# Kernel optimization log

Measured on AMD Instinct MI355X. Metric: run time of the kernel, lower is better.

The kernel has to match this reference:

```python
import jax, jax.numpy as jnp
import numpy as np

D_MODEL, N_HEADS, D_FF = 768, 12, 3072
D_HEAD = D_MODEL // N_HEADS
EPS = 1e-5


def layer_norm(x, g, b):
    mu = jnp.mean(x, axis=-1, keepdims=True)
    var = jnp.mean(jnp.square(x - mu), axis=-1, keepdims=True)
    return (x - mu) * jax.lax.rsqrt(var + EPS) * g + b


def setup_inputs() -> dict:
    key = jax.random.key(0)
    ks = jax.random.split(key, 8)
    B, T = 4, 2048
    s_in = 1.0 / np.sqrt(D_MODEL)
    s_ff = 1.0 / np.sqrt(D_FF)
    return {
        "x": jax.random.normal(ks[0], (B, T, D_MODEL), dtype=jnp.float32),
        "ln1_g": jnp.ones((D_MODEL,), jnp.float32),
        "ln1_b": jnp.zeros((D_MODEL,), jnp.float32),
        "qkv_w": jax.random.normal(ks[1], (D_MODEL, 3 * D_MODEL), jnp.float32) * s_in,
        "qkv_b": jnp.zeros((3 * D_MODEL,), jnp.float32),
        "attn_out_w": jax.random.normal(ks[2], (D_MODEL, D_MODEL), jnp.float32) * s_in,
        "attn_out_b": jnp.zeros((D_MODEL,), jnp.float32),
        "ln2_g": jnp.ones((D_MODEL,), jnp.float32),
        "ln2_b": jnp.zeros((D_MODEL,), jnp.float32),
        "ff1_w": jax.random.normal(ks[3], (D_MODEL, D_FF), jnp.float32) * s_in,
        "ff1_b": jnp.zeros((D_FF,), jnp.float32),
        "ff2_w": jax.random.normal(ks[4], (D_FF, D_MODEL), jnp.float32) * s_ff,
        "ff2_b": jnp.zeros((D_MODEL,), jnp.float32),
    }


def reference(x, ln1_g, ln1_b, qkv_w, qkv_b, attn_out_w, attn_out_b,
              ln2_g, ln2_b, ff1_w, ff1_b, ff2_w, ff2_b):
    B, T, D = x.shape
    h = layer_norm(x, ln1_g, ln1_b)
    qkv = h @ qkv_w + qkv_b                       # [B,T,3D]
    q, k, v = jnp.split(qkv, 3, axis=-1)
    def heads(t):  # [B,T,D] -> [B,H,T,dh]
        return t.reshape(B, T, N_HEADS, D_HEAD).transpose(0, 2, 1, 3)
    q, k, v = heads(q), heads(k), heads(v)
    scores = jnp.einsum('bhqd,bhkd->bhqk', q, k) / np.sqrt(D_HEAD)
    attn = jnp.einsum('bhqk,bhkd->bhqd', jax.nn.softmax(scores, axis=-1), v)
    attn = attn.transpose(0, 2, 1, 3).reshape(B, T, D)
    x = x + attn @ attn_out_w + attn_out_b
    h = layer_norm(x, ln2_g, ln2_b)
    ff = jax.nn.gelu(h @ ff1_w + ff1_b, approximate=True) @ ff2_w + ff2_b
    return x + ff
```

## Files before the change

### kernel.cpp

```cpp
#include <hip/hip_runtime.h>
#include <stdint.h>

typedef unsigned short ushort_t;
typedef unsigned int uint_t;

typedef __bf16 bf16x8 __attribute__((ext_vector_type(8)));
typedef float f32x4 __attribute__((ext_vector_type(4)));

#define DM 768
#define DFF 3072
#define NH 12
#define DH 64
#define TLEN 2048
#define BATCH 4
#define NROWS (BATCH * TLEN)
#define QKVW (3 * DM)
#define STG ((size_t)NROWS * DM)

#if __has_builtin(__builtin_amdgcn_exp2f)
#define EXP2(x) __builtin_amdgcn_exp2f(x)
#else
extern "C" __device__ float __ocml_native_exp2_f32(float);
#define EXP2(x) __ocml_native_exp2_f32(x)
#endif

__device__ __forceinline__ float b2f(ushort_t u) {
  union { uint_t i; float f; } c; c.i = ((uint_t)u) << 16; return c.f;
}
__device__ __forceinline__ ushort_t f2b(float f) {
  union { float f; uint_t i; } c; c.f = f;
  uint_t i = c.i;
  return (ushort_t)((i + 0x7fffu + ((i >> 16) & 1u)) >> 16);
}

__device__ __forceinline__ void gl_lds16(const ushort_t* g, ushort_t* l) {
  __builtin_amdgcn_global_load_lds(
      (const __attribute__((address_space(1))) uint_t*)g,
      (__attribute__((address_space(3))) uint_t*)l, 16, 0, 0);
}

__device__ __forceinline__ float gelu_f(float x) {
  float x2 = x * x;
  float c2n = -x * __builtin_fmaf(0.10294323f, x2, 2.3022082f);
  float t = EXP2(c2n);
  return x * __builtin_amdgcn_rcpf(1.0f + t);
}

__global__ __launch_bounds__(256) void detect_dtype(const ushort_t* __restrict__ x,
                                                    int* __restrict__ flag) {
  __shared__ int cnt[256];
  int c = 0;
  for (int i = threadIdx.x; i < 65536; i += 256)
    c += ((x[i] & 0x7F80u) == 0x7F80u) ? 1 : 0;
  cnt[threadIdx.x] = c;
  __syncthreads();
  for (int s = 128; s >= 1; s >>= 1) {
    if (threadIdx.x < s) cnt[threadIdx.x] += cnt[threadIdx.x + s];
    __syncthreads();
  }
  if (threadIdx.x == 0) flag[0] = (cnt[0] > 0) ? 1 : 0;
}

__global__ __launch_bounds__(256) void cvt_smalls(
    const void* s0, const void* s1, const void* s2, const void* s3,
    const void* s4, const void* s5, const void* s6, const void* s7,
    ushort_t* __restrict__ dst, const int* __restrict__ flag) {
  int f = flag[0];
  int i = blockIdx.x * 256 + threadIdx.x;
  if (i >= 9984) return;
  const void* src; int off;
  if (i < 768)       { src = s0; off = i; }
  else if (i < 1536) { src = s1; off = i - 768; }
  else if (i < 3840) { src = s2; off = i - 1536; }
  else if (i < 4608) { src = s3; off = i - 3840; }
  else if (i < 5376) { src = s4; off = i - 4608; }
  else if (i < 6144) { src = s5; off = i - 5376; }
  else if (i < 9216) { src = s6; off = i - 6144; }
  else               { src = s7; off = i - 9216; }
  dst[i] = f ? f2b(((const float*)src)[off]) : ((const ushort_t*)src)[off];
}

__global__ __launch_bounds__(256) void transpose_adapt(
    const void* __restrict__ inbase, long long inOff, ushort_t* __restrict__ out,
    int R, int C, int ldIn, const int* __restrict__ flag) {
  __shared__ alignas(16) ushort_t tile[32][33];
  int f = flag[0];
  const float* in32 = (const float*)inbase + inOff;
  const ushort_t* in16 = (const ushort_t*)inbase + inOff;
  int tc = blockIdx.x * 32, tr = blockIdx.y * 32;
  int lx = threadIdx.x & 31, ly = threadIdx.x >> 5;
#pragma unroll
  for (int i = 0; i < 32; i += 8) {
    size_t idx = (size_t)(tr + ly + i) * ldIn + tc + lx;
    tile[ly + i][lx] = f ? f2b(in32[idx]) : in16[idx];
  }
  __syncthreads();
#pragma unroll
  for (int i = 0; i < 32; i += 8)
    out[(size_t)(tc + ly + i) * R + tr + lx] = tile[lx][ly + i];
}

template <bool RAW>
__global__ __launch_bounds__(256) void ln_kernel(
    const void* __restrict__ xr, const ushort_t* __restrict__ g,
    const ushort_t* __restrict__ b, ushort_t* __restrict__ out,
    const int* __restrict__ flag) {
  int row = blockIdx.x * 4 + (threadIdx.x >> 6);
  int lane = threadIdx.x & 63;
  float v[12];
  if (RAW && flag[0]) {
    const float2* xp = (const float2*)((const float*)xr + (size_t)row * DM);
#pragma unroll
    for (int j = 0; j < 6; j++) {
      float2 t = xp[lane + 64 * j];
      v[2 * j] = t.x; v[2 * j + 1] = t.y;
    }
  } else {
    const uint_t* xu = (const uint_t*)((const ushort_t*)xr + (size_t)row * DM);
#pragma unroll
    for (int j = 0; j < 6; j++) {
      uint_t wv = xu[lane + 64 * j];
      v[2 * j] = b2f((ushort_t)(wv & 0xffffu));
      v[2 * j + 1] = b2f((ushort_t)(wv >> 16));
    }
  }
  float sum = 0.f, ss = 0.f;
#pragma unroll
  for (int k = 0; k < 12; k++) { sum += v[k]; ss += v[k] * v[k]; }
#pragma unroll
  for (int off = 32; off >= 1; off >>= 1) {
    sum += __shfl_xor(sum, off, 64);
    ss += __shfl_xor(ss, off, 64);
  }
  float mu = sum * (1.f / DM);
  float var = ss * (1.f / DM) - mu * mu;
  float rs = rsqrtf(var + 1e-5f);
  uint_t* ou = (uint_t*)(out + (size_t)row * DM);
  const uint_t* gu = (const uint_t*)g;
  const uint_t* bu = (const uint_t*)b;
#pragma unroll
  for (int j = 0; j < 6; j++) {
    int idx = lane + 64 * j;
    uint_t gw = gu[idx], bw = bu[idx];
    float o0 = (v[2 * j] - mu) * rs * b2f((ushort_t)(gw & 0xffffu)) + b2f((ushort_t)(bw & 0xffffu));
    float o1 = (v[2 * j + 1] - mu) * rs * b2f((ushort_t)(gw >> 16)) + b2f((ushort_t)(bw >> 16));
    ou[idx] = (uint_t)f2b(o0) | ((uint_t)f2b(o1) << 16);
  }
}

template <bool GELU, int RESMODE, int OUTMODE, int BM = 128, int BK = 32>
__global__ __launch_bounds__(256) void gemm_bt(
    const ushort_t* __restrict__ A, const ushort_t* __restrict__ BT,
    const ushort_t* __restrict__ bias, const void* __restrict__ res,
    void* __restrict__ outp, int M, int N, int K, int accum,
    const int* __restrict__ flagp) {
  constexpr int MI = (BM == 128) ? 4 : 2;
  constexpr int NI = 4;
  constexpr int KH = BK / 32;
  constexpr int LPS = (BM / 64 + 2) * KH;
  __shared__ alignas(16) ushort_t sA[2][BM * BK];
  __shared__ alignas(16) ushort_t sB[2][128 * BK];
  const int m0 = blockIdx.x * BM;
  const int n0 = blockIdx.y * 128;
  const int tid = threadIdx.x;
  const int w = tid >> 6, lane = tid & 63;
  const int quad = lane >> 4, l16 = lane & 15;
  const int wm = (w & 1) * (BM / 2);
  const int wn = (w >> 1) * 64;

  const f32x4 vz = {0.f, 0.f, 0.f, 0.f};
  f32x4 acc[MI][NI];
#pragma unroll
  for (int i = 0; i < MI; i++)
#pragma unroll
    for (int j = 0; j < NI; j++) acc[i][j] = vz;

  int colA;
  const ushort_t *gA, *gB;
  if constexpr (BK == 32) {
    colA = (((lane & 3) + ((lane >> 3) & 3)) & 3) * 8;
    gA = A + (size_t)(m0 + w * (BM / 4) + (lane >> 2)) * K + colA;
    gB = BT + (size_t)(n0 + w * 32 + (lane >> 2)) * K + colA;
  } else {
    colA = (((lane & 7) + (lane >> 3)) & 7) * 8;
    gA = A + (size_t)(m0 + w * 16 + (lane >> 3)) * K + colA;
    gB = BT + (size_t)(n0 + w * 32 + (lane >> 3)) * K + colA;
  }

  auto stage = [&](int k0, int buf) {
    if constexpr (BK == 32) {
      ushort_t* lA = &sA[buf][(w * (BM / 4)) * 32];
      ushort_t* lB = &sB[buf][(w * 32) * 32];
      gl_lds16(gA + k0, lA);
      if constexpr (BM == 128) gl_lds16(gA + k0 + (size_t)16 * K, lA + 16 * 32);
      gl_lds16(gB + k0, lB);
      gl_lds16(gB + k0 + (size_t)16 * K, lB + 16 * 32);
    } else {
      ushort_t* lA = &sA[buf][(w * 16) * 64];
      ushort_t* lB = &sB[buf][(w * 32) * 64];
      gl_lds16(gA + k0, lA);
      gl_lds16(gA + k0 + (size_t)8 * K, lA + 8 * 64);
#pragma unroll
      for (int i = 0; i < 4; i++)
        gl_lds16(gB + k0 + (size_t)(8 * i) * K, lB + i * 8 * 64);
    }
  };

  auto wait_lps = [&]() {
    if constexpr (LPS == 4) asm volatile("s_waitcnt vmcnt(4)" ::: "memory");
    else if constexpr (LPS == 3) asm volatile("s_waitcnt vmcnt(3)" ::: "memory");
    else asm volatile("s_waitcnt vmcnt(6)" ::: "memory");
  };

  const int nk = K / BK;
  stage(0, 0);
  stage(BK, 1);
  wait_lps();
  __builtin_amdgcn_s_barrier();

  for (int kt = 0; kt < nk; ++kt) {
    const int buf = kt & 1;
    bf16x8 af[KH][MI], bfr[KH][NI];
#pragma unroll
    for (int kk = 0; kk < KH; kk++) {
#pragma unroll
      for (int i = 0; i < MI; i++) {
        int ra = wm + i * 16 + l16;
        if constexpr (BK == 32)
          af[kk][i] = *(const bf16x8*)&sA[buf][ra * 32 + ((quad + 4 - ((ra >> 1) & 3)) & 3) * 8];
        else
          af[kk][i] = *(const bf16x8*)&sA[buf][ra * 64 + (((kk * 4 + quad) + 8 - (ra & 7)) & 7) * 8];
      }
#pragma unroll
      for (int i = 0; i < NI; i++) {
        int rb = wn + i * 16 + l16;
        if constexpr (BK == 32)
          bfr[kk][i] = *(const bf16x8*)&sB[buf][rb * 32 + ((quad + 4 - ((rb >> 1) & 3)) & 3) * 8];
        else
          bfr[kk][i] = *(const bf16x8*)&sB[buf][rb * 64 + (((kk * 4 + quad) + 8 - (rb & 7)) & 7) * 8];
      }
    }
    asm volatile("s_waitcnt lgkmcnt(0)" ::: "memory");
    __builtin_amdgcn_sched_barrier(0);
    __builtin_amdgcn_s_barrier();
    if (kt + 2 < nk) stage((kt + 2) * BK, buf);
#pragma unroll
    for (int kk = 0; kk < KH; kk++)
#pragma unroll
      for (int mi = 0; mi < MI; mi++)
#pragma unroll
        for (int ni = 0; ni < NI; ni++)
          acc[mi][ni] = __builtin_amdgcn_mfma_f32_16x16x32_bf16(af[kk][mi], bfr[kk][ni], acc[mi][ni], 0, 0, 0);
    if (kt + 2 < nk) {
      wait_lps();
      __builtin_amdgcn_s_barrier();
    } else if (kt + 1 < nk) {
      asm volatile("s_waitcnt vmcnt(0)" ::: "memory");
      __builtin_amdgcn_s_barrier();
    }
  }

  ushort_t* o16 = (ushort_t*)outp;
  float* o32 = (float*)outp;
  const int f32io = (OUTMODE == 1 || RESMODE == 2) ? flagp[0] : 0;
  float bsv[NI];
  int tyv[NI], hhv[NI], d7v[NI], d3v[NI], dv[NI];
#pragma unroll
  for (int ni = 0; ni < NI; ni++) {
    int col = n0 + wn + ni * 16 + l16;
    bsv[ni] = bias ? b2f(bias[col]) : 0.0f;
    if (OUTMODE == 2) {
      int ty = col >= 1536 ? 2 : (col >= 768 ? 1 : 0);
      int c2 = col - ty * 768;
      tyv[ni] = ty; hhv[ni] = c2 >> 6;
      dv[ni] = c2 & 63; d7v[ni] = c2 & 7; d3v[ni] = (c2 & 63) >> 3;
    }
  }
#pragma unroll
  for (int mi = 0; mi < MI; mi++) {
#pragma unroll
    for (int r = 0; r < 4; r++) {
      int row = m0 + wm + mi * 16 + quad * 4 + r;
      size_t rowb = 0; int kl = 0, klsw = 0, pl = 0;
      if (OUTMODE == 2) {
        int b = row >> 11, kt2 = (row >> 7) & 15;
        kl = row & 127;
        rowb = ((size_t)(b * NH) * 16 + kt2) * 8192;
        klsw = kl & 7;
        int k64 = kl & 63, m = k64 >> 4, qd = (k64 >> 2) & 3, r2 = k64 & 3;
        pl = (kl & 0x40) | ((m >> 1) << 5) | (qd << 3) | ((m & 1) << 2) | r2;
      }
#pragma unroll
      for (int ni = 0; ni < NI; ni++) {
        int col = n0 + wn + ni * 16 + l16;
        size_t idx = (size_t)row * N + col;
        float v = acc[mi][ni][r] + bsv[ni];
        if (GELU) v = gelu_f(v);
        if (RESMODE == 1) v += b2f(((const ushort_t*)res)[idx]);
        if (RESMODE == 2)
          v += f32io ? ((const float*)res)[idx] : b2f(((const ushort_t*)res)[idx]);
        if (OUTMODE == 1) {
          if (accum) v += f32io ? o32[idx] : b2f(o16[idx]);
          if (f32io) o32[idx] = v; else o16[idx] = f2b(v);
        } else if (OUTMODE == 2) {
          size_t tb = rowb + (size_t)hhv[ni] * 131072;
          size_t sidx;
          if (tyv[ni] == 2) {
            sidx = tb + (size_t)dv[ni] * 128 + (size_t)(((pl >> 3) ^ d7v[ni]) << 3) + (pl & 7);
          } else {
            if (tyv[ni] == 0) v *= 0.18033688011112042f;
            sidx = tb + (size_t)kl * 64 + (size_t)((d3v[ni] ^ klsw) << 3) + d7v[ni];
          }
          o16[(size_t)tyv[ni] * STG + sidx] = f2b(v);
        } else {
          o16[idx] = f2b(v);
        }
      }
    }
  }
}

__global__ __launch_bounds__(256) void attn_kernel(
    const ushort_t* __restrict__ qs, const ushort_t* __restrict__ ks,
    const ushort_t* __restrict__ vs, ushort_t* __restrict__ attnout) {
  __shared__ alignas(16) ushort_t sK[2][64 * 64];
  __shared__ alignas(16) ushort_t sV[2][64 * 64];
  const int bh = blockIdx.x;
  const int qt = blockIdx.y;
  const int tid = threadIdx.x;
  const int w = tid >> 6, lane = tid & 63;
  const int quad = lane >> 4, l16 = lane & 15;
  const int xsw = l16 & 7;
  const ushort_t* ktg0 = ks + (size_t)bh * 16 * 8192;
  const ushort_t* vtg0 = vs + (size_t)bh * 16 * 8192;

  {
    const ushort_t* qtg = qs + ((size_t)bh * 16 + qt) * 8192;
#pragma unroll
    for (int i = 0; i < 4; i++) {
      int off = (w * 4 + i) * 512;
      ushort_t* dst = (off < 4096) ? &sK[0][off] : &sK[1][off - 4096];
      gl_lds16(qtg + off + lane * 8, dst);
    }
  }
  __syncthreads();
  bf16x8 qf[2][2];
#pragma unroll
  for (int mq = 0; mq < 2; mq++) {
    int q = w * 32 + mq * 16 + l16;
    const ushort_t* sq = (q < 64) ? &sK[0][q * 64] : &sK[1][(q - 64) * 64];
#pragma unroll
    for (int c = 0; c < 2; c++)
      qf[mq][c] = *(const bf16x8*)&sq[((c * 4 + quad) ^ (q & 7)) * 8];
  }
  __syncthreads();

  bf16x8 onesf;
#pragma unroll
  for (int i = 0; i < 8; i++) onesf[i] = (__bf16)1.0f;

  f32x4 lsum[2];
  f32x4 oacc[2][4];
  const f32x4 vz = {0.f, 0.f, 0.f, 0.f};
#pragma unroll
  for (int mq = 0; mq < 2; mq++) {
    lsum[mq] = vz;
#pragma unroll
    for (int nd = 0; nd < 4; nd++) oacc[mq][nd] = vz;
  }

  auto stage = [&](int j, int buf) {
    const ushort_t* kg = ktg0 + (size_t)(j >> 1) * 8192 + (j & 1) * 4096;
    const ushort_t* vg = vtg0 + (size_t)(j >> 1) * 8192 + (j & 1) * 64;
#pragma unroll
    for (int i = 0; i < 2; i++) {
      int off = (w * 2 + i) * 512;
      gl_lds16(kg + off + lane * 8, &sK[buf][off]);
      gl_lds16(vg + (size_t)((w * 2 + i) * 8 + (lane >> 3)) * 128 + (lane & 7) * 8,
               &sV[buf][off]);
    }
  };

  stage(0, 0);

#pragma unroll 2
  for (int j = 0; j < 32; j++) {
    const int buf = j & 1;
    __syncthreads();
    if (j < 31) stage(j + 1, 1 - buf);

    f32x4 s[2][4];
    __builtin_amdgcn_s_setprio(1);
#pragma unroll
    for (int nk = 0; nk < 4; nk++) {
      int key = nk * 16 + l16;
      bf16x8 kf0 = *(const bf16x8*)&sK[buf][key * 64 + ((quad) ^ (key & 7)) * 8];
      bf16x8 kf1 = *(const bf16x8*)&sK[buf][key * 64 + ((4 + quad) ^ (key & 7)) * 8];
#pragma unroll
      for (int mq = 0; mq < 2; mq++) {
        s[mq][nk] = __builtin_amdgcn_mfma_f32_16x16x32_bf16(kf0, qf[mq][0], vz, 0, 0, 0);
        s[mq][nk] = __builtin_amdgcn_mfma_f32_16x16x32_bf16(kf1, qf[mq][1], s[mq][nk], 0, 0, 0);
      }
    }
    __builtin_amdgcn_s_setprio(0);

    bf16x8 pa[2][2];
#pragma unroll
    for (int mq = 0; mq < 2; mq++)
#pragma unroll
      for (int c = 0; c < 2; c++) {
        union { uint_t u[4]; bf16x8 v; } pk;
#pragma unroll
        for (int t = 0; t < 4; t++) {
          float lo = EXP2(s[mq][2 * c + (t >> 1)][(t & 1) * 2 + 0]);
          float hi = EXP2(s[mq][2 * c + (t >> 1)][(t & 1) * 2 + 1]);
          uint_t w32;
          asm("v_cvt_pk_bf16_f32 %0, %1, %2" : "=v"(w32) : "v"(lo), "v"(hi));
          pk.u[t] = w32;
        }
        pa[mq][c] = pk.v;
      }

    __builtin_amdgcn_s_setprio(1);
#pragma unroll
    for (int c = 0; c < 2; c++)
#pragma unroll
      for (int mq = 0; mq < 2; mq++)
        lsum[mq] = __builtin_amdgcn_mfma_f32_16x16x32_bf16(pa[mq][c], onesf, lsum[mq], 0, 0, 0);
#pragma unroll
    for (int c = 0; c < 2; c++)
#pragma unroll
      for (int nd = 0; nd < 4; nd++) {
        bf16x8 vf = *(const bf16x8*)&sV[buf][(nd * 16 + l16) * 64 + ((c * 4 + quad) ^ xsw) * 8];
#pragma unroll
        for (int mq = 0; mq < 2; mq++)
          oacc[mq][nd] = __builtin_amdgcn_mfma_f32_16x16x32_bf16(pa[mq][c], vf, oacc[mq][nd], 0, 0, 0);
      }
    __builtin_amdgcn_s_setprio(0);
  }

  const int b = bh / NH, h = bh - b * NH;
#pragma unroll
  for (int mq = 0; mq < 2; mq++) {
    float inv[4];
#pragma unroll
    for (int r = 0; r < 4; r++) inv[r] = __builtin_amdgcn_rcpf(lsum[mq][r]);
#pragma unroll
    for (int nd = 0; nd < 4; nd++) {
#pragma unroll
      for (int r = 0; r < 4; r++) {
        size_t row = (size_t)b * TLEN + qt * 128 + w * 32 + mq * 16 + quad * 4 + r;
        int col = h * DH + nd * 16 + l16;
        attnout[row * DM + col] = f2b(oacc[mq][nd][r] * inv[r]);
      }
    }
  }
}

extern "C" void kernel_launch(void* const* d_in, const int* in_sizes, int n_in,
                              void* d_out, int out_size, void* d_ws, size_t ws_size,
                              hipStream_t stream) {
  const void* x_r = d_in[0];
  const void* ln1_g_r = d_in[1];
  const void* ln1_b_r = d_in[2];
  const void* qkv_w_r = d_in[3];
  const void* qkv_b_r = d_in[4];
  const void* ao_w_r = d_in[5];
  const void* ao_b_r = d_in[6];
  const void* ln2_g_r = d_in[7];
  const void* ln2_b_r = d_in[8];
  const void* ff1_w_r = d_in[9];
  const void* ff1_b_r = d_in[10];
  const void* ff2_w_r = d_in[11];
  const void* ff2_b_r = d_in[12];

  int* flag = (int*)d_ws;
  ushort_t* base = (ushort_t*)d_ws + 128;
  const size_t RD = STG;

  const size_t elA = RD + RD + (size_t)NROWS * DFF + RD + (size_t)DM * DM + 9984;
  const bool pathA = ws_size >= elA * 2 + 4096;

  detect_dtype<<<1, 256, 0, stream>>>((const ushort_t*)x_r, flag);

  if (pathA) {
    ushort_t* x2   = base;
    ushort_t* h    = base + RD;
    ushort_t* big  = base + 2 * RD;
    ushort_t* aux  = big + (size_t)NROWS * DFF;
    ushort_t* wTa  = aux + RD;
    ushort_t* smalls = wTa + (size_t)DM * DM;
    ushort_t* wTq = aux;
    ushort_t* attnb = aux;
    ushort_t* wT2 = aux;
    ushort_t* wT3 = aux + (size_t)DFF * DM;
    ushort_t *g1 = smalls, *b1 = smalls + 768, *qb = smalls + 1536, *ab = smalls + 3840,
             *g2 = smalls + 4608, *b2 = smalls + 5376, *f1b = smalls + 6144, *f2bb = smalls + 9216;

    cvt_smalls<<<39, 256, 0, stream>>>(ln1_g_r, ln1_b_r, qkv_b_r, ao_b_r,
                                       ln2_g_r, ln2_b_r, ff1_b_r, ff2_b_r, smalls, flag);
    ln_kernel<true><<<NROWS / 4, 256, 0, stream>>>(x_r, g1, b1, h, flag);
    transpose_adapt<<<dim3(QKVW / 32, DM / 32), 256, 0, stream>>>(qkv_w_r, 0, wTq, DM, QKVW, QKVW, flag);
    gemm_bt<false, 0, 2, 64, 64><<<dim3(NROWS / 64, QKVW / 128), 256, 0, stream>>>(
        h, wTq, qb, nullptr, big, NROWS, QKVW, DM, 0, flag);
    attn_kernel<<<dim3(NH * BATCH, 16), 256, 0, stream>>>(big, big + STG, big + 2 * STG, attnb);
    transpose_adapt<<<dim3(DM / 32, DM / 32), 256, 0, stream>>>(ao_w_r, 0, wTa, DM, DM, DM, flag);
    gemm_bt<false, 2, 0, 64, 64><<<dim3(NROWS / 64, DM / 128), 256, 0, stream>>>(
        attnb, wTa, ab, x_r, x2, NROWS, DM, DM, 0, flag);
    ln_kernel<false><<<NROWS / 4, 256, 0, stream>>>(x2, g2, b2, h, flag);
    transpose_adapt<<<dim3(DFF / 32, DM / 32), 256, 0, stream>>>(ff1_w_r, 0, wT2, DM, DFF, DFF, flag);
    gemm_bt<true, 0, 0, 64, 64><<<dim3(NROWS / 64, DFF / 128), 256, 0, stream>>>(
        h, wT2, f1b, nullptr, big, NROWS, DFF, DM, 0, flag);
    transpose_adapt<<<dim3(DM / 32, DFF / 32), 256, 0, stream>>>(ff2_w_r, 0, wT3, DFF, DM, DM, flag);
    gemm_bt<false, 1, 1, 64, 64><<<dim3(NROWS / 64, DM / 128), 256, 0, stream>>>(
        big, wT3, f2bb, x2, d_out, NROWS, DM, DFF, 0, flag);
  } else {
    ushort_t* regA = base;
    ushort_t* regB = base + RD;
    ushort_t* slots = regB + (size_t)NROWS * QKVW;
    ushort_t* smalls = slots + (size_t)QKVW * DM + (size_t)DM * DM;
    ushort_t* h = regA, *attnb = regA, *h2 = regA;
    ushort_t* x2 = regB;
    ushort_t* ffq = regB + RD;
    ushort_t* wTq = slots;
    ushort_t* wTa = slots + (size_t)QKVW * DM;
    ushort_t* wT2 = slots;
    ushort_t* wT3 = slots + (size_t)1536 * DM;
    ushort_t *g1 = smalls, *b1 = smalls + 768, *qb = smalls + 1536, *ab = smalls + 3840,
             *g2 = smalls + 4608, *b2 = smalls + 5376, *f1b = smalls + 6144, *f2bb = smalls + 9216;

    cvt_smalls<<<39, 256, 0, stream>>>(ln1_g_r, ln1_b_r, qkv_b_r, ao_b_r,
                                       ln2_g_r, ln2_b_r, ff1_b_r, ff2_b_r, smalls, flag);
    ln_kernel<true><<<NROWS / 4, 256, 0, stream>>>(x_r, g1, b1, h, flag);
    transpose_adapt<<<dim3(QKVW / 32, DM / 32), 256, 0, stream>>>(qkv_w_r, 0, wTq, DM, QKVW, QKVW, flag);
    gemm_bt<false, 0, 2, 64, 64><<<dim3(NROWS / 64, QKVW / 128), 256, 0, stream>>>(
        h, wTq, qb, nullptr, regB, NROWS, QKVW, DM, 0, flag);
    attn_kernel<<<dim3(NH * BATCH, 16), 256, 0, stream>>>(regB, regB + STG, regB + 2 * STG, attnb);
    transpose_adapt<<<dim3(DM / 32, DM / 32), 256, 0, stream>>>(ao_w_r, 0, wTa, DM, DM, DM, flag);
    gemm_bt<false, 2, 0, 64, 64><<<dim3(NROWS / 64, DM / 128), 256, 0, stream>>>(
        attnb, wTa, ab, x_r, x2, NROWS, DM, DM, 0, flag);
    ln_kernel<false><<<NROWS / 4, 256, 0, stream>>>(x2, g2, b2, h2, flag);
    for (int q = 0; q < 2; q++) {
      transpose_adapt<<<dim3(1536 / 32, DM / 32), 256, 0, stream>>>(
          ff1_w_r, (long long)q * 1536, wT2, DM, 1536, DFF, flag);
      gemm_bt<true, 0, 0, 64, 64><<<dim3(NROWS / 64, 1536 / 128), 256, 0, stream>>>(
          h2, wT2, f1b + q * 1536, nullptr, ffq, NROWS, 1536, DM, 0, flag);
      transpose_adapt<<<dim3(DM / 32, 1536 / 32), 256, 0, stream>>>(
          ff2_w_r, (long long)q * 1536 * DM, wT3, 1536, DM, DM, flag);
      if (q == 0)
        gemm_bt<false, 1, 1, 64, 64><<<dim3(NROWS / 64, DM / 128), 256, 0, stream>>>(
            ffq, wT3, f2bb, x2, d_out, NROWS, DM, 1536, 0, flag);
      else
        gemm_bt<false, 0, 1, 64, 64><<<dim3(NROWS / 64, DM / 128), 256, 0, stream>>>(
            ffq, wT3, nullptr, nullptr, d_out, NROWS, DM, 1536, 1, flag);
    }
  }
}
```

Baseline: 420.1 us.

## Triple-buffer K/V tiles in attention with partial vmcnt waits

Attention K/V staging moves from a double buffer to a three-deep LDS ring, so tile j+2 is prefetched while tile j is consumed. The loop now waits with a partial s_waitcnt vmcnt(4) plus a raw s_barrier instead of __syncthreads, which keeps one stage's loads in flight across the barrier. This is meant to hide global-to-LDS latency. The cost is 50% more LDS per block, which may lower occupancy, plus the loss of the unroll-2 pragma and correctness that depends on exact vmcnt accounting.

```diff
diff --git a/kernel.cpp b/kernel.cpp
--- a/kernel.cpp
+++ b/kernel.cpp
@@ -323,8 +323,8 @@
 __global__ __launch_bounds__(256) void attn_kernel(
     const ushort_t* __restrict__ qs, const ushort_t* __restrict__ ks,
     const ushort_t* __restrict__ vs, ushort_t* __restrict__ attnout) {
-  __shared__ alignas(16) ushort_t sK[2][64 * 64];
-  __shared__ alignas(16) ushort_t sV[2][64 * 64];
+  __shared__ alignas(16) ushort_t sK[3][64 * 64];
+  __shared__ alignas(16) ushort_t sV[3][64 * 64];
   const int bh = blockIdx.x;
   const int qt = blockIdx.y;
   const int tid = threadIdx.x;
@@ -369,33 +369,40 @@
     for (int nd = 0; nd < 4; nd++) oacc[mq][nd] = vz;
   }
 
-  auto stage = [&](int j, int buf) {
+  auto stage = [&](int j, ushort_t* kb, ushort_t* vb) {
     const ushort_t* kg = ktg0 + (size_t)(j >> 1) * 8192 + (j & 1) * 4096;
     const ushort_t* vg = vtg0 + (size_t)(j >> 1) * 8192 + (j & 1) * 64;
 #pragma unroll
     for (int i = 0; i < 2; i++) {
       int off = (w * 2 + i) * 512;
-      gl_lds16(kg + off + lane * 8, &sK[buf][off]);
+      gl_lds16(kg + off + lane * 8, kb + off);
       gl_lds16(vg + (size_t)((w * 2 + i) * 8 + (lane >> 3)) * 128 + (lane & 7) * 8,
-               &sV[buf][off]);
+               vb + off);
     }
   };
 
-  stage(0, 0);
-
-#pragma unroll 2
+  stage(0, sK[0], sV[0]);
+  stage(1, sK[1], sV[1]);
+
+  ushort_t *kc = sK[0], *vc = sV[0];
+  ushort_t *kn = sK[1], *vn = sV[1];
+  ushort_t *kg2 = sK[2], *vg2 = sV[2];
+
   for (int j = 0; j < 32; j++) {
-    const int buf = j & 1;
-    __syncthreads();
-    if (j < 31) stage(j + 1, 1 - buf);
+    if (j < 31) asm volatile("s_waitcnt vmcnt(4)" ::: "memory");
+    else        asm volatile("s_waitcnt vmcnt(0)" ::: "memory");
+    asm volatile("s_waitcnt lgkmcnt(0)" ::: "memory");
+    __builtin_amdgcn_sched_barrier(0);
+    __builtin_amdgcn_s_barrier();
+    if (j < 30) stage(j + 2, kg2, vg2);
 
     f32x4 s[2][4];
     __builtin_amdgcn_s_setprio(1);
 #pragma unroll
     for (int nk = 0; nk < 4; nk++) {
       int key = nk * 16 + l16;
-      bf16x8 kf0 = *(const bf16x8*)&sK[buf][key * 64 + ((quad) ^ (key & 7)) * 8];
-      bf16x8 kf1 = *(const bf16x8*)&sK[buf][key * 64 + ((4 + quad) ^ (key & 7)) * 8];
+      bf16x8 kf0 = *(const bf16x8*)&kc[key * 64 + ((quad) ^ (key & 7)) * 8];
+      bf16x8 kf1 = *(const bf16x8*)&kc[key * 64 + ((4 + quad) ^ (key & 7)) * 8];
 #pragma unroll
       for (int mq = 0; mq < 2; mq++) {
         s[mq][nk] = __builtin_amdgcn_mfma_f32_16x16x32_bf16(kf0, qf[mq][0], vz, 0, 0, 0);
@@ -431,12 +438,16 @@
     for (int c = 0; c < 2; c++)
 #pragma unroll
       for (int nd = 0; nd < 4; nd++) {
-        bf16x8 vf = *(const bf16x8*)&sV[buf][(nd * 16 + l16) * 64 + ((c * 4 + quad) ^ xsw) * 8];
+        bf16x8 vf = *(const bf16x8*)&vc[(nd * 16 + l16) * 64 + ((c * 4 + quad) ^ xsw) * 8];
 #pragma unroll
         for (int mq = 0; mq < 2; mq++)
           oacc[mq][nd] = __builtin_amdgcn_mfma_f32_16x16x32_bf16(pa[mq][c], vf, oacc[mq][nd], 0, 0, 0);
       }
     __builtin_amdgcn_s_setprio(0);
+
+    ushort_t* t;
+    t = kc; kc = kn; kn = kg2; kg2 = t;
+    t = vc; vc = vn; vn = vg2; vg2 = t;
   }
 
   const int b = bh / NH, h = bh - b * NH;
```

Result: slower. 441.0 us (+5.0%).
